# Kernel optimization log

Hardware: AMD Instinct MI355X
Metric: run time of the kernel (lower is better)

Reference implementation:

```python
import jax, jax.numpy as jnp
import numpy as np

HEAD_SIZE = 64
N_EMBD = 1024
B, T = 8, 2048

def setup_inputs() -> dict:
    key = jax.random.key(0)
    kx, kq, kk, kv = jax.random.split(key, 4)
    x = jax.random.normal(kx, (B, T, N_EMBD), dtype=jnp.float32)
    s = 1.0 / np.sqrt(N_EMBD)
    Wq = jax.random.normal(kq, (N_EMBD, HEAD_SIZE), dtype=jnp.float32) * s
    Wk = jax.random.normal(kk, (N_EMBD, HEAD_SIZE), dtype=jnp.float32) * s
    Wv = jax.random.normal(kv, (N_EMBD, HEAD_SIZE), dtype=jnp.float32) * s
    return {"x": x, "Wq": Wq, "Wk": Wk, "Wv": Wv}

def reference(x, Wq, Wk, Wv):
    # x: [B,T,C]; project to q,k,v: [B,T,H]
    q = jnp.einsum('btc,ch->bth', x, Wq)
    k = jnp.einsum('btc,ch->bth', x, Wk)
    v = jnp.einsum('btc,ch->bth', x, Wv)
    scale = 1.0 / jnp.sqrt(jnp.asarray(HEAD_SIZE, dtype=x.dtype))
    wei = jnp.einsum('bth,bsh->bts', q, k) * scale  # [B,T,T]
    Tlen = x.shape[1]
    causal = jnp.tril(jnp.ones((Tlen, Tlen), dtype=bool))
    wei = jnp.where(causal[None, :, :], wei, jnp.asarray(-jnp.inf, dtype=wei.dtype))
    wei = jax.nn.softmax(wei, axis=-1)
    # dropout p=0.0 (eval) -> identity
    out = jnp.einsum('bts,bsh->bth', wei, v)  # [B,T,H]
    return out
```

## Files before the change

### kernel.cpp

```cpp
#include <hip/hip_runtime.h>
#include <math.h>

static constexpr int BN = 8;
static constexpr int TS = 2048;
static constexpr int CE = 1024;
static constexpr int HD = 64;

typedef __attribute__((ext_vector_type(8))) short bf16x8;
typedef __attribute__((ext_vector_type(4))) float f32x4;

__device__ __forceinline__ unsigned short f2bf(float f) {
    union { float f; unsigned u; } v; v.f = f;
    unsigned r = v.u + 0x7FFF + ((v.u >> 16) & 1);
    return (unsigned short)(r >> 16);
}

#define BARRIER() do { asm volatile("s_waitcnt lgkmcnt(0)" ::: "memory"); \
                       __builtin_amdgcn_s_barrier();                      \
                       asm volatile("" ::: "memory"); } while (0)

__global__ __launch_bounds__(256) void wt_kernel(
    const float* __restrict__ Wq, const float* __restrict__ Wk,
    const float* __restrict__ Wv, unsigned short* __restrict__ Wt)
{
    __shared__ float T[64 * 69];
    const int tid = threadIdx.x;
    const int m  = blockIdx.x >> 4;
    const int kt = blockIdx.x & 15;
    const float* W = (m == 0) ? Wq : (m == 1) ? Wk : Wv;
    const int k0 = kt * 64;

    #pragma unroll
    for (int it = 0; it < 4; ++it) {
        int idx = tid + it * 256;
        int r = idx >> 4, nq = idx & 15;
        float4 v = *(const float4*)(W + (long)(k0 + r) * HD + nq * 4);
        T[r * 69 + nq * 4 + 0] = v.x;
        T[r * 69 + nq * 4 + 1] = v.y;
        T[r * 69 + nq * 4 + 2] = v.z;
        T[r * 69 + nq * 4 + 3] = v.w;
    }
    __syncthreads();
    #pragma unroll
    for (int it = 0; it < 2; ++it) {
        int idx = tid + it * 256;
        int n = idx >> 3, kq = idx & 7;
        unsigned short h[8];
        #pragma unroll
        for (int s = 0; s < 8; ++s)
            h[s] = f2bf(T[(kq * 8 + s) * 69 + n]);
        *(uint4*)(Wt + (long)(m * 64 + n) * CE + k0 + kq * 8) = *(uint4*)h;
    }
}

static constexpr int NTI = CE / 64;

__global__ __launch_bounds__(256) void qkv_mfma_kernel(
    const float* __restrict__ x, const unsigned short* __restrict__ Wt,
    unsigned short* __restrict__ qo, unsigned short* __restrict__ ko,
    unsigned short* __restrict__ vo)
{
    __shared__ __align__(16) unsigned short xL0[32 * 64];
    __shared__ __align__(16) unsigned short xL1[32 * 64];

    const int tid = threadIdx.x;
    const int l  = tid & 63, w = tid >> 6;
    const int lr = l & 15,  h = l >> 4;
    const long row0 = (long)blockIdx.x * 32;

    const int sr = tid >> 3;
    const int sq = tid & 7;
    const int slot = sq ^ (sr & 7);
    const float* xgr = x + (row0 + sr) * CE + sq * 8;
    unsigned short* xw0 = &xL0[sr * 64 + slot * 8];
    unsigned short* xw1 = &xL1[sr * 64 + slot * 8];

    const unsigned short* wb0 = Wt + (long)(w * 48 + 0  + lr) * CE + 8 * h;
    const unsigned short* wb1 = Wt + (long)(w * 48 + 16 + lr) * CE + 8 * h;
    const unsigned short* wb2 = Wt + (long)(w * 48 + 32 + lr) * CE + 8 * h;

    const int sw0 = ((0 + h) ^ (lr & 7)) * 8;
    const int sw1 = ((4 + h) ^ (lr & 7)) * 8;

    f32x4 acc[2][3];
    #pragma unroll
    for (int i = 0; i < 2; ++i)
        #pragma unroll
        for (int j = 0; j < 3; ++j)
            acc[i][j] = (f32x4){0.f, 0.f, 0.f, 0.f};

    bf16x8 bA[6], bB[6];
    float4 Ro0, Ro1, Re0, Re1;

    {
        float4 t0 = *(const float4*)(xgr);
        float4 t1 = *(const float4*)(xgr + 4);
        Ro0 = *(const float4*)(xgr + 64);
        Ro1 = *(const float4*)(xgr + 68);
        Re0 = *(const float4*)(xgr + 128);
        Re1 = *(const float4*)(xgr + 132);
        #pragma unroll
        for (int j = 0; j < 3; ++j) {
            const unsigned short* wbj = (j == 0) ? wb0 : (j == 1) ? wb1 : wb2;
            bA[j * 2 + 0] = *(const bf16x8*)(wbj);
            bA[j * 2 + 1] = *(const bf16x8*)(wbj + 32);
        }
        unsigned short hh[8] = { f2bf(t0.x), f2bf(t0.y), f2bf(t0.z), f2bf(t0.w),
                                 f2bf(t1.x), f2bf(t1.y), f2bf(t1.z), f2bf(t1.w) };
        *(uint4*)xw0 = *(uint4*)hh;
    }
    BARRIER();

    #define STAGE(dst, r0, r1) do {                                          \
        unsigned short hh[8] = { f2bf((r0).x), f2bf((r0).y), f2bf((r0).z),   \
                                 f2bf((r0).w), f2bf((r1).x), f2bf((r1).y),   \
                                 f2bf((r1).z), f2bf((r1).w) };               \
        *(uint4*)(dst) = *(uint4*)hh; } while (0)

    #define LOADW(arr, t) do {                                               \
        (arr)[0] = *(const bf16x8*)(wb0 + (t) * 64);                         \
        (arr)[1] = *(const bf16x8*)(wb0 + (t) * 64 + 32);                    \
        (arr)[2] = *(const bf16x8*)(wb1 + (t) * 64);                         \
        (arr)[3] = *(const bf16x8*)(wb1 + (t) * 64 + 32);                    \
        (arr)[4] = *(const bf16x8*)(wb2 + (t) * 64);                         \
        (arr)[5] = *(const bf16x8*)(wb2 + (t) * 64 + 32);  } while (0)

    #define COMPUTE(buf, b) do {                                             \
        _Pragma("unroll")                                                    \
        for (int kk = 0; kk < 2; ++kk) {                                     \
            const int ss = kk ? sw1 : sw0;                                   \
            bf16x8 a0 = *(const bf16x8*)(&(buf)[lr * 64 + ss]);              \
            bf16x8 a1 = *(const bf16x8*)(&(buf)[(16 + lr) * 64 + ss]);       \
            _Pragma("unroll")                                                \
            for (int j = 0; j < 3; ++j) {                                    \
                acc[0][j] = __builtin_amdgcn_mfma_f32_16x16x32_bf16(         \
                    a0, (b)[j * 2 + kk], acc[0][j], 0, 0, 0);                \
                acc[1][j] = __builtin_amdgcn_mfma_f32_16x16x32_bf16(         \
                    a1, (b)[j * 2 + kk], acc[1][j], 0, 0, 0);                \
            }                                                                \
        } } while (0)

    for (int t = 0; t < NTI; t += 2) {
        STAGE(xw1, Ro0, Ro1);
        if (t + 3 < NTI) {
            Ro0 = *(const float4*)(xgr + (t + 3) * 64);
            Ro1 = *(const float4*)(xgr + (t + 3) * 64 + 4);
        }
        LOADW(bB, t + 1);
        COMPUTE(xL0, bA);
        BARRIER();

        if (t + 2 < NTI) {
            STAGE(xw0, Re0, Re1);
            if (t + 4 < NTI) {
                Re0 = *(const float4*)(xgr + (t + 4) * 64);
                Re1 = *(const float4*)(xgr + (t + 4) * 64 + 4);
            }
            LOADW(bA, t + 2);
        }
        COMPUTE(xL1, bB);
        if (t + 2 < NTI) BARRIER();
    }

    #pragma unroll
    for (int j = 0; j < 3; ++j) {
        const int n0 = w * 48 + 16 * j;
        if (n0 < 128) {
            unsigned short* outp = (n0 < 64) ? qo : ko;
            const int h0 = (n0 & 63) + lr;
            #pragma unroll
            for (int i = 0; i < 2; ++i)
                #pragma unroll
                for (int r = 0; r < 4; ++r) {
                    long rowg = row0 + 16 * i + h * 4 + r;
                    outp[rowg * HD + h0] = f2bf(acc[i][j][r]);
                }
        } else {
            const int d  = (n0 - 128) + lr;
            const int bb = (int)(row0 >> 11);
            const int t0 = (int)(row0 & 2047) + h * 4;
            #pragma unroll
            for (int i = 0; i < 2; ++i) {
                unsigned short h4[4];
                #pragma unroll
                for (int r = 0; r < 4; ++r) h4[r] = f2bf(acc[i][j][r]);
                *(uint2*)(vo + (((long)(bb * 64 + d)) << 11) + t0 + 16 * i) = *(uint2*)h4;
            }
        }
    }
    #undef STAGE
    #undef LOADW
    #undef COMPUTE
}

__global__ __launch_bounds__(256) void attn_mfma_kernel(
    const unsigned short* __restrict__ qg,
    const unsigned short* __restrict__ kg,
    const unsigned short* __restrict__ vtg,
    float* __restrict__ out)
{
    __shared__ unsigned short Pl[4][32 * 72];
    __shared__ float Ow[4][32 * 64];
    __shared__ float Ml[4][32], Ll[4][32];

    const int tid = threadIdx.x;
    const int w  = tid >> 6;
    const int l  = tid & 63;
    const int lr = l & 15, h = l >> 4;
    const int b  = blockIdx.x >> 5;
    const int pr = blockIdx.x & 31;

    const unsigned short* qB = qg  + (long)b * TS * HD;
    const unsigned short* kB = kg  + (long)b * TS * HD;
    const unsigned short* vT = vtg + (long)b * HD * TS;
    float* outB = out + (long)b * TS * HD;

    unsigned short* Pw = &Pl[w][0];

    for (int half = 0; half < 2; ++half) {
        const int qt = half ? (63 - pr) : pr;
        const int q0 = qt * 32;
        const int NT = (qt + 2) >> 1;

        bf16x8 Qf[2][2];
        #pragma unroll
        for (int qf = 0; qf < 2; ++qf)
            #pragma unroll
            for (int ks = 0; ks < 2; ++ks)
                Qf[qf][ks] = *(const bf16x8*)(qB + (q0 + 16 * qf + lr) * HD + 32 * ks + 8 * h);

        f32x4 O[2][4];
        #pragma unroll
        for (int rf = 0; rf < 2; ++rf)
            #pragma unroll
            for (int cf = 0; cf < 4; ++cf)
                O[rf][cf] = (f32x4){0.f, 0.f, 0.f, 0.f};
        float mrow[2] = {-1e30f, -1e30f};
        float lrow[2] = {0.f, 0.f};

        for (int kt = w; kt < NT; kt += 4) {
            const int key0 = kt * 64;
            bf16x8 Kf[4][2], Vf[4][2];
            #pragma unroll
            for (int kf = 0; kf < 4; ++kf)
                #pragma unroll
                for (int ks = 0; ks < 2; ++ks)
                    Kf[kf][ks] = *(const bf16x8*)(kB + (key0 + 16 * kf + lr) * HD + 32 * ks + 8 * h);
            #pragma unroll
            for (int cf = 0; cf < 4; ++cf)
                #pragma unroll
                for (int ks = 0; ks < 2; ++ks)
                    Vf[cf][ks] = *(const bf16x8*)(vT + (16 * cf + lr) * TS + key0 + 32 * ks + 8 * h);

            f32x4 st[4][2];
            #pragma unroll
            for (int kf = 0; kf < 4; ++kf)
                #pragma unroll
                for (int qf = 0; qf < 2; ++qf)
                    st[kf][qf] = (f32x4){0.f, 0.f, 0.f, 0.f};
            #pragma unroll
            for (int ks = 0; ks < 2; ++ks)
                #pragma unroll
                for (int kf = 0; kf < 4; ++kf)
                    #pragma unroll
                    for (int qf = 0; qf < 2; ++qf)
                        st[kf][qf] = __builtin_amdgcn_mfma_f32_16x16x32_bf16(
                            Kf[kf][ks], Qf[qf][ks], st[kf][qf], 0, 0, 0);

            const bool lastt = (kt == NT - 1);
            float alpha[2];
            #pragma unroll
            for (int qf = 0; qf < 2; ++qf) {
                const int qrow = q0 + 16 * qf + lr;
                float tm = -1e30f;
                #pragma unroll
                for (int kf = 0; kf < 4; ++kf)
                    #pragma unroll
                    for (int r = 0; r < 4; ++r) {
                        float sv = st[kf][qf][r] * 0.125f;
                        if (lastt && (key0 + 16 * kf + 4 * h + r) > qrow) sv = -1e30f;
                        st[kf][qf][r] = sv;
                        tm = fmaxf(tm, sv);
                    }
                tm = fmaxf(tm, __shfl_xor(tm, 16));
                tm = fmaxf(tm, __shfl_xor(tm, 32));
                const float mn = fmaxf(mrow[qf], tm);
                alpha[qf] = __expf(mrow[qf] - mn);
                mrow[qf] = mn;
                float rs = 0.f;
                #pragma unroll
                for (int kf = 0; kf < 4; ++kf)
                    #pragma unroll
                    for (int r = 0; r < 4; ++r) {
                        float p = __expf(st[kf][qf][r] - mn);
                        st[kf][qf][r] = p;
                        rs += p;
                    }
                rs += __shfl_xor(rs, 16);
                rs += __shfl_xor(rs, 32);
                lrow[qf] = lrow[qf] * alpha[qf] + rs;
                #pragma unroll
                for (int kf = 0; kf < 4; ++kf) {
                    unsigned a01 = (unsigned)f2bf(st[kf][qf][0]) |
                                   ((unsigned)f2bf(st[kf][qf][1]) << 16);
                    unsigned a23 = (unsigned)f2bf(st[kf][qf][2]) |
                                   ((unsigned)f2bf(st[kf][qf][3]) << 16);
                    unsigned short* pp = Pw + (16 * qf + lr) * 72 + 16 * kf + 4 * h;
                    *(unsigned*)(pp)     = a01;
                    *(unsigned*)(pp + 2) = a23;
                }
            }

            #pragma unroll
            for (int rf = 0; rf < 2; ++rf)
                #pragma unroll
                for (int r = 0; r < 4; ++r) {
                    float aO = __shfl(alpha[rf], 4 * h + r);
                    #pragma unroll
                    for (int cf = 0; cf < 4; ++cf)
                        O[rf][cf][r] *= aO;
                }

            bf16x8 pa[2][2];
            #pragma unroll
            for (int rf = 0; rf < 2; ++rf)
                #pragma unroll
                for (int ks = 0; ks < 2; ++ks)
                    pa[rf][ks] = *(const bf16x8*)(Pw + (16 * rf + lr) * 72 + 32 * ks + 8 * h);
            #pragma unroll
            for (int ks = 0; ks < 2; ++ks)
                #pragma unroll
                for (int rf = 0; rf < 2; ++rf)
                    #pragma unroll
                    for (int cf = 0; cf < 4; ++cf)
                        O[rf][cf] = __builtin_amdgcn_mfma_f32_16x16x32_bf16(
                            pa[rf][ks], Vf[cf][ks], O[rf][cf], 0, 0, 0);
        }

        #pragma unroll
        for (int rf = 0; rf < 2; ++rf)
            #pragma unroll
            for (int cf = 0; cf < 4; ++cf)
                #pragma unroll
                for (int r = 0; r < 4; ++r)
                    Ow[w][(16 * rf + 4 * h + r) * 64 + 16 * cf + lr] = O[rf][cf][r];
        if (h == 0) {
            #pragma unroll
            for (int qf = 0; qf < 2; ++qf) {
                Ml[w][16 * qf + lr] = mrow[qf];
                Ll[w][16 * qf + lr] = lrow[qf];
            }
        }
        __syncthreads();

        {
            const int q  = tid >> 3;
            const int d0 = (tid & 7) * 8;
            float mM = -1e30f;
            #pragma unroll
            for (int w2 = 0; w2 < 4; ++w2) mM = fmaxf(mM, Ml[w2][q]);
            float lS = 0.f;
            float a8[8] = {0.f,0.f,0.f,0.f,0.f,0.f,0.f,0.f};
            #pragma unroll
            for (int w2 = 0; w2 < 4; ++w2) {
                float sc = __expf(Ml[w2][q] - mM);
                lS += Ll[w2][q] * sc;
                #pragma unroll
                for (int e = 0; e < 8; ++e)
                    a8[e] += sc * Ow[w2][q * 64 + d0 + e];
            }
            const float inv = 1.f / lS;
            float4 o1 = {a8[0]*inv, a8[1]*inv, a8[2]*inv, a8[3]*inv};
            float4 o2 = {a8[4]*inv, a8[5]*inv, a8[6]*inv, a8[7]*inv};
            *(float4*)(outB + (long)(q0 + q) * HD + d0)     = o1;
            *(float4*)(outB + (long)(q0 + q) * HD + d0 + 4) = o2;
        }
        __syncthreads();
    }
}

extern "C" void kernel_launch(void* const* d_in, const int* in_sizes, int n_in,
                              void* d_out, int out_size, void* d_ws, size_t ws_size,
                              hipStream_t stream) {
    const float* x  = (const float*)d_in[0];
    const float* Wq = (const float*)d_in[1];
    const float* Wk = (const float*)d_in[2];
    const float* Wv = (const float*)d_in[3];
    float* out = (float*)d_out;

    const size_t nqkv = (size_t)BN * TS * HD;
    unsigned short* qb = (unsigned short*)d_ws;
    unsigned short* kb = qb + nqkv;
    unsigned short* vt = kb + nqkv;

    unsigned short* Wt = (unsigned short*)d_out;

    wt_kernel<<<48, 256, 0, stream>>>(Wq, Wk, Wv, Wt);
    qkv_mfma_kernel<<<(BN * TS) / 32, 256, 0, stream>>>(x, Wt, qb, kb, vt);
    attn_mfma_kernel<<<BN * 32, 256, 0, stream>>>(qb, kb, vt, out);
}
```

Measured before the change: 60.02 us.

## Load x fragments directly from global in QKV projection, dropping LDS staging

The QKV projection kernel no longer stages bf16-converted x tiles through double-buffered shared memory with barriers. Each wave now loads its own fp32 x fragments straight from global memory into registers and packs them to bf16 right before the MFMAs, with register double-buffering of both x and W. This removes LDS writes and reads and all block barriers from the main loop. In exchange, all four waves in a block read the same x rows, so global and L2 traffic for the large x tensor grows about fourfold, and register pressure rises.

```diff
diff --git a/kernel.cpp b/kernel.cpp
--- a/kernel.cpp
+++ b/kernel.cpp
@@ -15,9 +15,14 @@
     return (unsigned short)(r >> 16);
 }
 
-#define BARRIER() do { asm volatile("s_waitcnt lgkmcnt(0)" ::: "memory"); \
-                       __builtin_amdgcn_s_barrier();                      \
-                       asm volatile("" ::: "memory"); } while (0)
+__device__ __forceinline__ bf16x8 pack8(const float4& a, const float4& b) {
+    union { unsigned u[4]; bf16x8 v; } r;
+    r.u[0] = (unsigned)f2bf(a.x) | ((unsigned)f2bf(a.y) << 16);
+    r.u[1] = (unsigned)f2bf(a.z) | ((unsigned)f2bf(a.w) << 16);
+    r.u[2] = (unsigned)f2bf(b.x) | ((unsigned)f2bf(b.y) << 16);
+    r.u[3] = (unsigned)f2bf(b.z) | ((unsigned)f2bf(b.w) << 16);
+    return r.v;
+}
 
 __global__ __launch_bounds__(256) void wt_kernel(
     const float* __restrict__ Wq, const float* __restrict__ Wk,
@@ -60,28 +65,17 @@
     unsigned short* __restrict__ qo, unsigned short* __restrict__ ko,
     unsigned short* __restrict__ vo)
 {
-    __shared__ __align__(16) unsigned short xL0[32 * 64];
-    __shared__ __align__(16) unsigned short xL1[32 * 64];
-
     const int tid = threadIdx.x;
     const int l  = tid & 63, w = tid >> 6;
     const int lr = l & 15,  h = l >> 4;
     const long row0 = (long)blockIdx.x * 32;
 
-    const int sr = tid >> 3;
-    const int sq = tid & 7;
-    const int slot = sq ^ (sr & 7);
-    const float* xgr = x + (row0 + sr) * CE + sq * 8;
-    unsigned short* xw0 = &xL0[sr * 64 + slot * 8];
-    unsigned short* xw1 = &xL1[sr * 64 + slot * 8];
-
+    const float* xb0 = x + (row0 + lr) * CE + 8 * h;
+    const float* xb1 = x + (row0 + 16 + lr) * CE + 8 * h;
     const unsigned short* wb0 = Wt + (long)(w * 48 + 0  + lr) * CE + 8 * h;
     const unsigned short* wb1 = Wt + (long)(w * 48 + 16 + lr) * CE + 8 * h;
     const unsigned short* wb2 = Wt + (long)(w * 48 + 32 + lr) * CE + 8 * h;
 
-    const int sw0 = ((0 + h) ^ (lr & 7)) * 8;
-    const int sw1 = ((4 + h) ^ (lr & 7)) * 8;
-
     f32x4 acc[2][3];
     #pragma unroll
     for (int i = 0; i < 2; ++i)
@@ -89,78 +83,55 @@
         for (int j = 0; j < 3; ++j)
             acc[i][j] = (f32x4){0.f, 0.f, 0.f, 0.f};
 
-    bf16x8 bA[6], bB[6];
-    float4 Ro0, Ro1, Re0, Re1;
-
-    {
-        float4 t0 = *(const float4*)(xgr);
-        float4 t1 = *(const float4*)(xgr + 4);
-        Ro0 = *(const float4*)(xgr + 64);
-        Ro1 = *(const float4*)(xgr + 68);
-        Re0 = *(const float4*)(xgr + 128);
-        Re1 = *(const float4*)(xgr + 132);
-        #pragma unroll
-        for (int j = 0; j < 3; ++j) {
-            const unsigned short* wbj = (j == 0) ? wb0 : (j == 1) ? wb1 : wb2;
-            bA[j * 2 + 0] = *(const bf16x8*)(wbj);
-            bA[j * 2 + 1] = *(const bf16x8*)(wbj + 32);
-        }
-        unsigned short hh[8] = { f2bf(t0.x), f2bf(t0.y), f2bf(t0.z), f2bf(t0.w),
-                                 f2bf(t1.x), f2bf(t1.y), f2bf(t1.z), f2bf(t1.w) };
-        *(uint4*)xw0 = *(uint4*)hh;
-    }
-    BARRIER();
-
-    #define STAGE(dst, r0, r1) do {                                          \
-        unsigned short hh[8] = { f2bf((r0).x), f2bf((r0).y), f2bf((r0).z),   \
-                                 f2bf((r0).w), f2bf((r1).x), f2bf((r1).y),   \
-                                 f2bf((r1).z), f2bf((r1).w) };               \
-        *(uint4*)(dst) = *(uint4*)hh; } while (0)
-
-    #define LOADW(arr, t) do {                                               \
-        (arr)[0] = *(const bf16x8*)(wb0 + (t) * 64);                         \
-        (arr)[1] = *(const bf16x8*)(wb0 + (t) * 64 + 32);                    \
-        (arr)[2] = *(const bf16x8*)(wb1 + (t) * 64);                         \
-        (arr)[3] = *(const bf16x8*)(wb1 + (t) * 64 + 32);                    \
-        (arr)[4] = *(const bf16x8*)(wb2 + (t) * 64);                         \
-        (arr)[5] = *(const bf16x8*)(wb2 + (t) * 64 + 32);  } while (0)
-
-    #define COMPUTE(buf, b) do {                                             \
-        _Pragma("unroll")                                                    \
-        for (int kk = 0; kk < 2; ++kk) {                                     \
-            const int ss = kk ? sw1 : sw0;                                   \
-            bf16x8 a0 = *(const bf16x8*)(&(buf)[lr * 64 + ss]);              \
-            bf16x8 a1 = *(const bf16x8*)(&(buf)[(16 + lr) * 64 + ss]);       \
-            _Pragma("unroll")                                                \
-            for (int j = 0; j < 3; ++j) {                                    \
-                acc[0][j] = __builtin_amdgcn_mfma_f32_16x16x32_bf16(         \
-                    a0, (b)[j * 2 + kk], acc[0][j], 0, 0, 0);                \
-                acc[1][j] = __builtin_amdgcn_mfma_f32_16x16x32_bf16(         \
-                    a1, (b)[j * 2 + kk], acc[1][j], 0, 0, 0);                \
-            }                                                                \
+    float4 XA[2][2][2], XB[2][2][2];
+    bf16x8 WA[6], WB[6];
+
+    #define LOADX(X, t) do {                                                  \
+        _Pragma("unroll")                                                     \
+        for (int i = 0; i < 2; ++i) {                                         \
+            const float* xb = i ? xb1 : xb0;                                  \
+            _Pragma("unroll")                                                 \
+            for (int kk = 0; kk < 2; ++kk) {                                  \
+                (X)[i][kk][0] = *(const float4*)(xb + (t) * 64 + kk * 32);    \
+                (X)[i][kk][1] = *(const float4*)(xb + (t) * 64 + kk * 32 + 4);\
+            }                                                                 \
         } } while (0)
 
+    #define LOADW(Bv, t) do {                                                 \
+        (Bv)[0] = *(const bf16x8*)(wb0 + (t) * 64);                           \
+        (Bv)[1] = *(const bf16x8*)(wb0 + (t) * 64 + 32);                      \
+        (Bv)[2] = *(const bf16x8*)(wb1 + (t) * 64);                           \
+        (Bv)[3] = *(const bf16x8*)(wb1 + (t) * 64 + 32);                      \
+        (Bv)[4] = *(const bf16x8*)(wb2 + (t) * 64);                           \
+        (Bv)[5] = *(const bf16x8*)(wb2 + (t) * 64 + 32);  } while (0)
+
+    #define STEP(X, Bv) do {                                                  \
+        _Pragma("unroll")                                                     \
+        for (int kk = 0; kk < 2; ++kk) {                                      \
+            bf16x8 a0 = pack8((X)[0][kk][0], (X)[0][kk][1]);                  \
+            bf16x8 a1 = pack8((X)[1][kk][0], (X)[1][kk][1]);                  \
+            _Pragma("unroll")                                                 \
+            for (int j = 0; j < 3; ++j) {                                     \
+                acc[0][j] = __builtin_amdgcn_mfma_f32_16x16x32_bf16(          \
+                    a0, (Bv)[j * 2 + kk], acc[0][j], 0, 0, 0);                \
+                acc[1][j] = __builtin_amdgcn_mfma_f32_16x16x32_bf16(          \
+                    a1, (Bv)[j * 2 + kk], acc[1][j], 0, 0, 0);                \
+            }                                                                 \
+        } } while (0)
+
+    LOADX(XA, 0);
+    LOADW(WA, 0);
+
+    #pragma unroll
     for (int t = 0; t < NTI; t += 2) {
-        STAGE(xw1, Ro0, Ro1);
-        if (t + 3 < NTI) {
-            Ro0 = *(const float4*)(xgr + (t + 3) * 64);
-            Ro1 = *(const float4*)(xgr + (t + 3) * 64 + 4);
-        }
-        LOADW(bB, t + 1);
-        COMPUTE(xL0, bA);
-        BARRIER();
-
-        if (t + 2 < NTI) {
-            STAGE(xw0, Re0, Re1);
-            if (t + 4 < NTI) {
-                Re0 = *(const float4*)(xgr + (t + 4) * 64);
-                Re1 = *(const float4*)(xgr + (t + 4) * 64 + 4);
-            }
-            LOADW(bA, t + 2);
-        }
-        COMPUTE(xL1, bB);
-        if (t + 2 < NTI) BARRIER();
-    }
+        if (t + 1 < NTI) { LOADX(XB, t + 1); LOADW(WB, t + 1); }
+        STEP(XA, WA);
+        if (t + 2 < NTI) { LOADX(XA, t + 2); LOADW(WA, t + 2); }
+        if (t + 1 < NTI) STEP(XB, WB);
+    }
+    #undef LOADX
+    #undef LOADW
+    #undef STEP
 
     #pragma unroll
     for (int j = 0; j < 3; ++j) {
@@ -188,9 +159,6 @@
             }
         }
     }
-    #undef STAGE
-    #undef LOADW
-    #undef COMPUTE
 }
 
 __global__ __launch_bounds__(256) void attn_mfma_kernel(
```

Result: slower. 83.74 us (+39.5%).
